# Performance work log

Measured on AMD Instinct MI355X. Metric: run time of the kernel, lower is better.

## Reference

```python
import jax, jax.numpy as jnp
import numpy as np

WIN = 9  # window size per spatial dim (default [9,9,9] for 3D)


def _window_sum(x):
    # Depthwise conv with an all-ones [9,9,9] kernel, stride 1, zero pad 4
    # == sliding-window box sum. lax.reduce_window is the efficient, exact form.
    pad = WIN // 2
    return jax.lax.reduce_window(
        x, 0.0, jax.lax.add,
        window_dimensions=(1, 1, WIN, WIN, WIN),
        window_strides=(1, 1, 1, 1, 1),
        padding=((0, 0), (0, 0), (pad, pad), (pad, pad), (pad, pad)),
    )


def setup_inputs() -> dict:
    key = jax.random.key(0)
    k1, k2 = jax.random.split(key)
    shape = (2, 1, 160, 160, 160)  # [B, C, D, H, W]
    y_true = jax.random.normal(k1, shape, dtype=jnp.float32)
    y_pred = jax.random.normal(k2, shape, dtype=jnp.float32)
    return {"y_true": y_true, "y_pred": y_pred}


def reference(y_true, y_pred):
    Ii, Ji = y_true, y_pred
    win_size = jnp.asarray(WIN ** 3, dtype=Ii.dtype)  # 729

    I2 = Ii * Ii
    J2 = Ji * Ji
    IJ = Ii * Ji

    I_sum = _window_sum(Ii)
    J_sum = _window_sum(Ji)
    I2_sum = _window_sum(I2)
    J2_sum = _window_sum(J2)
    IJ_sum = _window_sum(IJ)

    u_I = I_sum / win_size
    u_J = J_sum / win_size

    cross = IJ_sum - u_J * I_sum - u_I * J_sum + u_I * u_J * win_size
    I_var = I2_sum - 2.0 * u_I * I_sum + u_I * u_I * win_size
    J_var = J2_sum - 2.0 * u_J * J_sum + u_J * u_J * win_size

    cc = cross * cross / (I_var * J_var + 1e-05)
    # mean over spatial dims [2,3,4] -> [B,C], then mean -> scalar
    return (1.0 - jnp.mean(cc, axis=(2, 3, 4))).mean()
```

## Files before the change

kernel.cpp:

```cpp
#include <hip/hip_runtime.h>


typedef float floatx2 __attribute__((ext_vector_type(2)));

constexpr int W = 160, H = 160, D = 160;
constexpr int SLICE = W * H;
constexpr int NVOX  = W * H * D;
constexpr int BATCH = 2;
constexpr int FROW  = 5 * W;
constexpr float RW  = 1.0f / 729.0f;

constexpr int TPB_ZX = 320;
constexpr int ROWS_PB = 8;
constexpr int XGZ   = W / 4;
constexpr int CHZ   = 5, NCHZ = D / CHZ;
constexpr int NTUP_ZX = BATCH * NCHZ * H;
constexpr int NBLK_ZX = NTUP_ZX / ROWS_PB;
constexpr int LROW  = 168;

constexpr int TPB_Y = 256;
constexpr int XGY   = W / 8;
constexpr int CHY   = 2, NCHY = H / CHY;
constexpr int NTH_Y = BATCH * D * NCHY * XGY;
constexpr int NBLK_Y = NTH_Y / TPB_Y;

__device__ inline unsigned int pk4(float a, float b, float c, float d) {
    unsigned int u = 0;
    u = __builtin_amdgcn_cvt_pk_fp8_f32(a, b, u, false);
    u = __builtin_amdgcn_cvt_pk_fp8_f32(c, d, u, true);
    return u;
}
__device__ inline void up8(uint2 v, float* o) {
    floatx2 t;
    t = __builtin_amdgcn_cvt_pk_f32_fp8(v.x, false); o[0] = t[0]; o[1] = t[1];
    t = __builtin_amdgcn_cvt_pk_f32_fp8(v.x, true);  o[2] = t[0]; o[3] = t[1];
    t = __builtin_amdgcn_cvt_pk_f32_fp8(v.y, false); o[4] = t[0]; o[5] = t[1];
    t = __builtin_amdgcn_cvt_pk_f32_fp8(v.y, true);  o[6] = t[0]; o[7] = t[1];
}

__global__ __launch_bounds__(TPB_ZX) void pass_zx(const float* __restrict__ I,
                                                  const float* __restrict__ J,
                                                  unsigned char* __restrict__ outA) {
    __shared__ float lds[ROWS_PB][5][LROW];

    int tid = threadIdx.x;
    int r  = tid / XGZ;
    int xg = tid % XGZ;
    int tuple = blockIdx.x * ROWS_PB + r;
    int y = tuple % H;
    int c = (tuple / H) % NCHZ;
    int b = tuple / (H * NCHZ);
    int x0 = xg * 4;
    const float* Ib = I + (size_t)b * NVOX + y * W + x0;
    const float* Jb = J + (size_t)b * NVOX + y * W + x0;
    unsigned char* ob = outA + ((size_t)b * D * H + y) * FROW + x0;

    if (xg == 0) {
#pragma unroll
        for (int f = 0; f < 5; ++f) {
            lds[r][f][0] = 0.f; lds[r][f][1] = 0.f;
            lds[r][f][2] = 0.f; lds[r][f][3] = 0.f;
        }
    }
    if (xg == XGZ - 1) {
#pragma unroll
        for (int f = 0; f < 5; ++f) {
            lds[r][f][164] = 0.f; lds[r][f][165] = 0.f;
            lds[r][f][166] = 0.f; lds[r][f][167] = 0.f;
        }
    }

    float s[5][4];
#pragma unroll
    for (int f = 0; f < 5; ++f)
#pragma unroll
        for (int i = 0; i < 4; ++i) s[f][i] = 0.f;

    auto addS = [&](int zz) {
        float4 a = *(const float4*)(Ib + (size_t)zz * SLICE);
        float4 bb = *(const float4*)(Jb + (size_t)zz * SLICE);
        float av[4] = {a.x, a.y, a.z, a.w};
        float bv[4] = {bb.x, bb.y, bb.z, bb.w};
#pragma unroll
        for (int i = 0; i < 4; ++i) {
            float x = av[i], yv = bv[i];
            s[0][i] += x; s[1][i] += yv;
            s[2][i] += x * x; s[3][i] += yv * yv; s[4][i] += x * yv;
        }
    };

    int z0 = c * CHZ;
    for (int zz = (z0 - 4 < 0 ? 0 : z0 - 4); zz <= z0 + 4; ++zz) addS(zz);

    for (int dz = 0; dz < CHZ; ++dz) {
        int z = z0 + dz;
        int za = z + 5, zs = z - 4;
        bool ha = za < D, hs = zs >= 0;
        float4 Az = ha ? *(const float4*)(Ib + (size_t)za * SLICE) : make_float4(0.f, 0.f, 0.f, 0.f);
        float4 Bz = ha ? *(const float4*)(Jb + (size_t)za * SLICE) : make_float4(0.f, 0.f, 0.f, 0.f);
        float4 As = hs ? *(const float4*)(Ib + (size_t)zs * SLICE) : make_float4(0.f, 0.f, 0.f, 0.f);
        float4 Bs = hs ? *(const float4*)(Jb + (size_t)zs * SLICE) : make_float4(0.f, 0.f, 0.f, 0.f);

#pragma unroll
        for (int f = 0; f < 5; ++f)
            *(float4*)&lds[r][f][4 + x0] = make_float4(s[f][0], s[f][1], s[f][2], s[f][3]);
        __syncthreads();

        unsigned char* op = ob + (size_t)z * (H * FROW);
#pragma unroll
        for (int f = 0; f < 5; ++f) {
            float4 Lv = *(const float4*)&lds[r][f][x0];
            float4 Rv = *(const float4*)&lds[r][f][x0 + 8];
            float p0 = Lv.x;
            float p1 = p0 + Lv.y;
            float p2 = p1 + Lv.z;
            float p3 = p2 + Lv.w;
            float p4 = p3 + s[f][0];
            float p5 = p4 + s[f][1];
            float p6 = p5 + s[f][2];
            float p7 = p6 + s[f][3];
            float p8 = p7 + Rv.x;
            float p9 = p8 + Rv.y;
            float p10 = p9 + Rv.z;
            float p11 = p10 + Rv.w;
            *(unsigned int*)(op + f * W) = pk4(p8, p9 - p0, p10 - p1, p11 - p2);
        }
        __syncthreads();

        float ae[4] = {Az.x, Az.y, Az.z, Az.w};
        float be[4] = {Bz.x, Bz.y, Bz.z, Bz.w};
        float al[4] = {As.x, As.y, As.z, As.w};
        float bl[4] = {Bs.x, Bs.y, Bs.z, Bs.w};
#pragma unroll
        for (int i = 0; i < 4; ++i) {
            s[0][i] += ae[i] - al[i];
            s[1][i] += be[i] - bl[i];
            s[2][i] += ae[i] * ae[i] - al[i] * al[i];
            s[3][i] += be[i] * be[i] - bl[i] * bl[i];
            s[4][i] += ae[i] * be[i] - al[i] * bl[i];
        }
    }
}

__global__ __launch_bounds__(TPB_Y) void pass_y(const unsigned char* __restrict__ A,
                                                double* __restrict__ partials) {
    int tid = threadIdx.x;
    int t = blockIdx.x * TPB_Y + tid;
    int xg = t % XGY;
    int tup = t / XGY;
    int yc = tup % NCHY;
    int z  = (tup / NCHY) % D;
    int b  = tup / (NCHY * D);
    int x0 = xg * 8;
    const unsigned char* __restrict__ base =
        A + (size_t)(b * D + z) * H * FROW + x0;
    int y0 = yc * CHY;

    float s[5][8];
#pragma unroll
    for (int f = 0; f < 5; ++f)
#pragma unroll
        for (int i = 0; i < 8; ++i) s[f][i] = 0.f;

    int ylo = y0 - 4 < 0 ? 0 : y0 - 4;
    int yhi = y0 + 4 > H - 1 ? H - 1 : y0 + 4;
    for (int yy = ylo; yy <= yhi; ++yy) {
        const unsigned char* rp = base + (size_t)yy * FROW;
#pragma unroll
        for (int f = 0; f < 5; ++f) {
            uint2 v = *(const uint2*)(rp + f * W);
            float u[8]; up8(v, u);
#pragma unroll
            for (int i = 0; i < 8; ++i) s[f][i] += u[i];
        }
    }

    double acc = 0.0;
#pragma unroll
    for (int dy = 0; dy < CHY; ++dy) {
        int ye = y0 + dy + 5, yl = y0 + dy - 4;
        bool he = ye < H, hl = yl >= 0;
        uint2 pe[5], pl[5];
        const unsigned char* pre = base + (size_t)(he ? ye : 0) * FROW;
        const unsigned char* prl = base + (size_t)(hl ? yl : 0) * FROW;
#pragma unroll
        for (int f = 0; f < 5; ++f) {
            pe[f] = he ? *(const uint2*)(pre + f * W) : make_uint2(0u, 0u);
            pl[f] = hl ? *(const uint2*)(prl + f * W) : make_uint2(0u, 0u);
        }

        float rowcc = 0.f;
#pragma unroll
        for (int i = 0; i < 8; ++i) {
            float Is = s[0][i], Js = s[1][i];
            float I2s = s[2][i], J2s = s[3][i], IJs = s[4][i];
            float tI = RW * Is;
            float cross = __builtin_fmaf(-tI, Js, IJs);
            float Iv    = __builtin_fmaf(-tI, Is, I2s);
            float Jv    = __builtin_fmaf(-(RW * Js), Js, J2s);
            float den   = __builtin_fmaf(Iv, Jv, 1e-5f);
            rowcc = __builtin_fmaf(cross * cross, __builtin_amdgcn_rcpf(den), rowcc);
        }
        acc += (double)rowcc;

#pragma unroll
        for (int f = 0; f < 5; ++f) {
            float ue[8], ul[8];
            up8(pe[f], ue); up8(pl[f], ul);
#pragma unroll
            for (int i = 0; i < 8; ++i) s[f][i] += ue[i] - ul[i];
        }
    }

#pragma unroll
    for (int off = 32; off > 0; off >>= 1) acc += __shfl_down(acc, off);
    __shared__ double sm[TPB_Y / 64];
    if ((tid & 63) == 0) sm[tid >> 6] = acc;
    __syncthreads();
    if (tid == 0) {
        double tt = 0.0;
#pragma unroll
        for (int i = 0; i < TPB_Y / 64; ++i) tt += sm[i];
        partials[blockIdx.x] = tt;
    }
}

__global__ __launch_bounds__(256) void finalize(const double* __restrict__ p,
                                                float* __restrict__ out) {
    double v = 0.0;
    for (int i = threadIdx.x; i < NBLK_Y; i += 256) v += p[i];
#pragma unroll
    for (int off = 32; off > 0; off >>= 1) v += __shfl_down(v, off);
    __shared__ double sm[4];
    int lane = threadIdx.x & 63, wid = threadIdx.x >> 6;
    if (lane == 0) sm[wid] = v;
    __syncthreads();
    if (threadIdx.x == 0) {
        double tt = 0.0;
#pragma unroll
        for (int i = 0; i < 4; ++i) tt += sm[i];
        out[0] = (float)(1.0 - tt / (double)((double)BATCH * (double)NVOX));
    }
}

extern "C" void kernel_launch(void* const* d_in, const int* in_sizes, int n_in,
                              void* d_out, int out_size, void* d_ws, size_t ws_size,
                              hipStream_t stream) {
    const float* I = (const float*)d_in[0];
    const float* J = (const float*)d_in[1];
    float* out = (float*)d_out;

    size_t bufsz = ((size_t)BATCH * 5 * NVOX + 255) / 256 * 256;
    unsigned char* bufA = (unsigned char*)d_ws;
    double* partials = (double*)(bufA + bufsz);

    pass_zx<<<NBLK_ZX, TPB_ZX, 0, stream>>>(I, J, bufA);
    pass_y<<<NBLK_Y, TPB_Y, 0, stream>>>(bufA, partials);
    finalize<<<1, 256, 0, stream>>>(partials, out);
}
```

Before: 63.80 us.

## Use bf16 double-buffered LDS in zx pass and retile y pass to 4-wide

In the z/x pass, the shared-memory staging of running sums becomes bf16 in a double buffer indexed by dz parity, which removes the second barrier per step and halves LDS traffic. The dz loop is also fully unrolled. In the y pass each thread now covers 4 x-columns and 4 output rows instead of 8 columns and 2 rows, using 32-bit fp8 loads. Neighbour sums read back in bf16 add rounding error on top of the existing fp8 intermediate, and the smaller y-pass loads may reduce memory efficiency.

```diff
diff --git a/kernel.cpp b/kernel.cpp
--- a/kernel.cpp
+++ b/kernel.cpp
@@ -19,9 +19,9 @@
 constexpr int LROW  = 168;
 
 constexpr int TPB_Y = 256;
-constexpr int XGY   = W / 8;
-constexpr int CHY   = 2, NCHY = H / CHY;
-constexpr int NTH_Y = BATCH * D * NCHY * XGY;
+constexpr int XGY4  = W / 4;
+constexpr int CHY   = 4, NCHY = H / CHY;
+constexpr int NTH_Y = BATCH * D * NCHY * XGY4;
 constexpr int NBLK_Y = NTH_Y / TPB_Y;
 
 __device__ inline unsigned int pk4(float a, float b, float c, float d) {
@@ -30,18 +30,30 @@
     u = __builtin_amdgcn_cvt_pk_fp8_f32(c, d, u, true);
     return u;
 }
-__device__ inline void up8(uint2 v, float* o) {
+__device__ inline void up4(unsigned int v, float* o) {
     floatx2 t;
-    t = __builtin_amdgcn_cvt_pk_f32_fp8(v.x, false); o[0] = t[0]; o[1] = t[1];
-    t = __builtin_amdgcn_cvt_pk_f32_fp8(v.x, true);  o[2] = t[0]; o[3] = t[1];
-    t = __builtin_amdgcn_cvt_pk_f32_fp8(v.y, false); o[4] = t[0]; o[5] = t[1];
-    t = __builtin_amdgcn_cvt_pk_f32_fp8(v.y, true);  o[6] = t[0]; o[7] = t[1];
+    t = __builtin_amdgcn_cvt_pk_f32_fp8(v, false); o[0] = t[0]; o[1] = t[1];
+    t = __builtin_amdgcn_cvt_pk_f32_fp8(v, true);  o[2] = t[0]; o[3] = t[1];
+}
+__device__ inline unsigned short f2bf(float f) {
+    unsigned int u = __builtin_bit_cast(unsigned int, f);
+    u += 0x7fffu + ((u >> 16) & 1u);
+    return (unsigned short)(u >> 16);
+}
+__device__ inline unsigned int bfpack2(float lo, float hi) {
+    return (unsigned int)f2bf(lo) | ((unsigned int)f2bf(hi) << 16);
+}
+__device__ inline float bflo(unsigned int u) {
+    return __builtin_bit_cast(float, u << 16);
+}
+__device__ inline float bfhi(unsigned int u) {
+    return __builtin_bit_cast(float, u & 0xffff0000u);
 }
 
 __global__ __launch_bounds__(TPB_ZX) void pass_zx(const float* __restrict__ I,
                                                   const float* __restrict__ J,
                                                   unsigned char* __restrict__ outA) {
-    __shared__ float lds[ROWS_PB][5][LROW];
+    __shared__ unsigned short xw[2][ROWS_PB][5][LROW];
 
     int tid = threadIdx.x;
     int r  = tid / XGZ;
@@ -57,17 +69,21 @@
 
     if (xg == 0) {
 #pragma unroll
-        for (int f = 0; f < 5; ++f) {
-            lds[r][f][0] = 0.f; lds[r][f][1] = 0.f;
-            lds[r][f][2] = 0.f; lds[r][f][3] = 0.f;
-        }
+        for (int p = 0; p < 2; ++p)
+#pragma unroll
+            for (int f = 0; f < 5; ++f) {
+                xw[p][r][f][0] = 0; xw[p][r][f][1] = 0;
+                xw[p][r][f][2] = 0; xw[p][r][f][3] = 0;
+            }
     }
     if (xg == XGZ - 1) {
 #pragma unroll
-        for (int f = 0; f < 5; ++f) {
-            lds[r][f][164] = 0.f; lds[r][f][165] = 0.f;
-            lds[r][f][166] = 0.f; lds[r][f][167] = 0.f;
-        }
+        for (int p = 0; p < 2; ++p)
+#pragma unroll
+            for (int f = 0; f < 5; ++f) {
+                xw[p][r][f][164] = 0; xw[p][r][f][165] = 0;
+                xw[p][r][f][166] = 0; xw[p][r][f][167] = 0;
+            }
     }
 
     float s[5][4];
@@ -92,6 +108,7 @@
     int z0 = c * CHZ;
     for (int zz = (z0 - 4 < 0 ? 0 : z0 - 4); zz <= z0 + 4; ++zz) addS(zz);
 
+#pragma unroll
     for (int dz = 0; dz < CHZ; ++dz) {
         int z = z0 + dz;
         int za = z + 5, zs = z - 4;
@@ -101,31 +118,37 @@
         float4 As = hs ? *(const float4*)(Ib + (size_t)zs * SLICE) : make_float4(0.f, 0.f, 0.f, 0.f);
         float4 Bs = hs ? *(const float4*)(Jb + (size_t)zs * SLICE) : make_float4(0.f, 0.f, 0.f, 0.f);
 
-#pragma unroll
-        for (int f = 0; f < 5; ++f)
-            *(float4*)&lds[r][f][4 + x0] = make_float4(s[f][0], s[f][1], s[f][2], s[f][3]);
+        int p = dz & 1;
+#pragma unroll
+        for (int f = 0; f < 5; ++f) {
+            uint2 w;
+            w.x = bfpack2(s[f][0], s[f][1]);
+            w.y = bfpack2(s[f][2], s[f][3]);
+            *(uint2*)&xw[p][r][f][4 + x0] = w;
+        }
         __syncthreads();
 
         unsigned char* op = ob + (size_t)z * (H * FROW);
 #pragma unroll
         for (int f = 0; f < 5; ++f) {
-            float4 Lv = *(const float4*)&lds[r][f][x0];
-            float4 Rv = *(const float4*)&lds[r][f][x0 + 8];
-            float p0 = Lv.x;
-            float p1 = p0 + Lv.y;
-            float p2 = p1 + Lv.z;
-            float p3 = p2 + Lv.w;
+            uint2 Lv = *(const uint2*)&xw[p][r][f][x0];
+            uint2 Rv = *(const uint2*)&xw[p][r][f][x0 + 8];
+            float l0 = bflo(Lv.x), l1 = bfhi(Lv.x), l2 = bflo(Lv.y), l3 = bfhi(Lv.y);
+            float r0 = bflo(Rv.x), r1 = bfhi(Rv.x), r2 = bflo(Rv.y), r3 = bfhi(Rv.y);
+            float p0 = l0;
+            float p1 = p0 + l1;
+            float p2 = p1 + l2;
+            float p3 = p2 + l3;
             float p4 = p3 + s[f][0];
             float p5 = p4 + s[f][1];
             float p6 = p5 + s[f][2];
             float p7 = p6 + s[f][3];
-            float p8 = p7 + Rv.x;
-            float p9 = p8 + Rv.y;
-            float p10 = p9 + Rv.z;
-            float p11 = p10 + Rv.w;
+            float p8 = p7 + r0;
+            float p9 = p8 + r1;
+            float p10 = p9 + r2;
+            float p11 = p10 + r3;
             *(unsigned int*)(op + f * W) = pk4(p8, p9 - p0, p10 - p1, p11 - p2);
         }
-        __syncthreads();
 
         float ae[4] = {Az.x, Az.y, Az.z, Az.w};
         float be[4] = {Bz.x, Bz.y, Bz.z, Bz.w};
@@ -146,21 +169,21 @@
                                                 double* __restrict__ partials) {
     int tid = threadIdx.x;
     int t = blockIdx.x * TPB_Y + tid;
-    int xg = t % XGY;
-    int tup = t / XGY;
+    int xg = t % XGY4;
+    int tup = t / XGY4;
     int yc = tup % NCHY;
     int z  = (tup / NCHY) % D;
     int b  = tup / (NCHY * D);
-    int x0 = xg * 8;
+    int x0 = xg * 4;
     const unsigned char* __restrict__ base =
         A + (size_t)(b * D + z) * H * FROW + x0;
     int y0 = yc * CHY;
 
-    float s[5][8];
+    float s[5][4];
 #pragma unroll
     for (int f = 0; f < 5; ++f)
 #pragma unroll
-        for (int i = 0; i < 8; ++i) s[f][i] = 0.f;
+        for (int i = 0; i < 4; ++i) s[f][i] = 0.f;
 
     int ylo = y0 - 4 < 0 ? 0 : y0 - 4;
     int yhi = y0 + 4 > H - 1 ? H - 1 : y0 + 4;
@@ -168,10 +191,10 @@
         const unsigned char* rp = base + (size_t)yy * FROW;
 #pragma unroll
         for (int f = 0; f < 5; ++f) {
-            uint2 v = *(const uint2*)(rp + f * W);
-            float u[8]; up8(v, u);
-#pragma unroll
-            for (int i = 0; i < 8; ++i) s[f][i] += u[i];
+            unsigned int v = *(const unsigned int*)(rp + f * W);
+            float u[4]; up4(v, u);
+#pragma unroll
+            for (int i = 0; i < 4; ++i) s[f][i] += u[i];
         }
     }
 
@@ -180,18 +203,18 @@
     for (int dy = 0; dy < CHY; ++dy) {
         int ye = y0 + dy + 5, yl = y0 + dy - 4;
         bool he = ye < H, hl = yl >= 0;
-        uint2 pe[5], pl[5];
+        unsigned int pe[5], pl[5];
         const unsigned char* pre = base + (size_t)(he ? ye : 0) * FROW;
         const unsigned char* prl = base + (size_t)(hl ? yl : 0) * FROW;
 #pragma unroll
         for (int f = 0; f < 5; ++f) {
-            pe[f] = he ? *(const uint2*)(pre + f * W) : make_uint2(0u, 0u);
-            pl[f] = hl ? *(const uint2*)(prl + f * W) : make_uint2(0u, 0u);
+            pe[f] = he ? *(const unsigned int*)(pre + f * W) : 0u;
+            pl[f] = hl ? *(const unsigned int*)(prl + f * W) : 0u;
         }
 
         float rowcc = 0.f;
 #pragma unroll
-        for (int i = 0; i < 8; ++i) {
+        for (int i = 0; i < 4; ++i) {
             float Is = s[0][i], Js = s[1][i];
             float I2s = s[2][i], J2s = s[3][i], IJs = s[4][i];
             float tI = RW * Is;
@@ -205,10 +228,10 @@
 
 #pragma unroll
         for (int f = 0; f < 5; ++f) {
-            float ue[8], ul[8];
-            up8(pe[f], ue); up8(pl[f], ul);
-#pragma unroll
-            for (int i = 0; i < 8; ++i) s[f][i] += ue[i] - ul[i];
+            float ue[4], ul[4];
+            up4(pe[f], ue); up4(pl[f], ul);
+#pragma unroll
+            for (int i = 0; i < 4; ++i) s[f][i] += ue[i] - ul[i];
         }
     }
 
```

Result: slower. 67.60 us (+6.0%).
